# Kernel tuning notes

Hardware: AMD Instinct MI355X
Metric: run time of the kernel (lower is better)

The kernel has to match this reference:

```python
import jax, jax.numpy as jnp
import numpy as np

N, E, B, H, L, T = 50000, 800000, 1000, 256, 5, 128
BN_EPS = 1e-5

def _bn(x, g, b):
    # training-mode batchnorm over node axis, biased variance (torch semantics)
    mu = jnp.mean(x, axis=0)
    var = jnp.mean(jnp.square(x - mu), axis=0)
    return (x - mu) * jax.lax.rsqrt(var + BN_EPS) * g + b

def setup_inputs() -> dict:
    key = jax.random.key(0)
    ks = jax.random.split(key, 12)
    s = lambda fan: 1.0 / np.sqrt(fan)
    inp = {}
    inp["x_atom"] = jax.random.normal(ks[0], (N, 9), jnp.float32)
    inp["x_pe"] = jax.random.normal(ks[1], (N, 8), jnp.float32)
    inp["edge_index"] = jax.random.randint(ks[2], (2, E), 0, N, dtype=jnp.int64)
    inp["batch"] = jnp.sort(jax.random.randint(ks[3], (N,), 0, B, dtype=jnp.int64))
    inp["ae_w"] = jax.random.normal(ks[4], (9, H), jnp.float32) * s(9)
    inp["ae_b"] = jnp.zeros((H,), jnp.float32)
    inp["pe_w"] = jax.random.normal(ks[5], (8, H), jnp.float32) * s(8)
    inp["pe_b"] = jnp.zeros((H,), jnp.float32)
    inp["w1"] = jax.random.normal(ks[6], (L, H, H), jnp.float32) * s(H)
    inp["b1"] = jnp.zeros((L, H), jnp.float32)
    inp["g1"] = jnp.ones((L, H), jnp.float32)
    inp["be1"] = jnp.zeros((L, H), jnp.float32)
    inp["w2"] = jax.random.normal(ks[7], (L, H, H), jnp.float32) * s(H)
    inp["b2"] = jnp.zeros((L, H), jnp.float32)
    inp["bng"] = jnp.ones((L, H), jnp.float32)
    inp["bnb"] = jnp.zeros((L, H), jnp.float32)
    inp["cl1_w"] = jax.random.normal(ks[8], (H, H), jnp.float32) * s(H)
    inp["cl1_b"] = jnp.zeros((H,), jnp.float32)
    inp["clg"] = jnp.ones((H,), jnp.float32)
    inp["clb"] = jnp.zeros((H,), jnp.float32)
    inp["cl2_w"] = jax.random.normal(ks[9], (H, T), jnp.float32) * s(H)
    inp["cl2_b"] = jnp.zeros((T,), jnp.float32)
    return inp

def reference(x_atom, x_pe, edge_index, batch, ae_w, ae_b, pe_w, pe_b,
              w1, b1, g1, be1, w2, b2, bng, bnb,
              cl1_w, cl1_b, clg, clb, cl2_w, cl2_b):
    src, dst = edge_index[0], edge_index[1]
    h = x_atom @ ae_w + ae_b + x_pe @ pe_w + pe_b  # (N, H)
    for i in range(L):
        # GINConv (eps=0): (1+eps)*x + sum_{j in N(i)} x_j, then MLP
        agg = jax.ops.segment_sum(h[src], dst, num_segments=N)
        z = h + agg
        z = z @ w1[i] + b1[i]
        z = jax.nn.relu(_bn(z, g1[i], be1[i]))
        z = z @ w2[i] + b2[i]
        # outer BN + ReLU (dropout is identity in eval)
        h = jax.nn.relu(_bn(z, bng[i], bnb[i]))
    # global mean pool per graph
    sums = jax.ops.segment_sum(h, batch, num_segments=B)
    counts = jax.ops.segment_sum(jnp.ones((N,), h.dtype), batch, num_segments=B)
    pooled = sums / jnp.maximum(counts, 1.0)[:, None]  # (B, H)
    z = pooled @ cl1_w + cl1_b
    z = jax.nn.relu(_bn(z, clg, clb))
    logits = z @ cl2_w + cl2_b  # (B, T)
    return logits
```

## Files before the change

kernel.cpp:

```cpp
#include <hip/hip_runtime.h>
#include <hip/hip_bf16.h>
#include <stdint.h>

#define HH 256
#define BN_EPS 1e-5f
#define CHUNK 256
#define NSLOT 12

static inline int cdiv(int a, int b) { return (a + b - 1) / b; }

typedef _Float16 f16x8 __attribute__((ext_vector_type(8)));
typedef __attribute__((ext_vector_type(4))) float f32x4;

__device__ __forceinline__ unsigned short f2h(float f) {
    _Float16 h = (_Float16)f;
    unsigned short u;
    __builtin_memcpy(&u, &h, 2);
    return u;
}
__device__ __forceinline__ float h2f(unsigned short u) {
    _Float16 h;
    __builtin_memcpy(&h, &u, 2);
    return (float)h;
}

__device__ __forceinline__ void gload16(const void* g, void* lds) {
    __builtin_amdgcn_global_load_lds((const __attribute__((address_space(1))) unsigned int*)g,
                                     (__attribute__((address_space(3))) unsigned int*)lds, 16, 0, 0);
}

__device__ __forceinline__ void bn_derive(const float* __restrict__ stats, const float* __restrict__ g,
                                          const float* __restrict__ b, float invM, int c,
                                          float& sc, float& sh) {
    float mu = stats[c] * invM;
    float var = stats[HH + c] * invM - mu * mu;
    float rstd = rsqrtf(var + BN_EPS);
    sc = rstd * g[c];
    sh = b[c] - mu * sc;
}

__global__ void embed_kernel(const float* __restrict__ xa, const float* __restrict__ xp,
                             const float* __restrict__ aw, const float* __restrict__ ab,
                             const float* __restrict__ pw, const float* __restrict__ pb,
                             unsigned short* __restrict__ h, int N) {
    int n = blockIdx.x;
    int c = threadIdx.x;
    if (n >= N) return;
    float acc = ab[c] + pb[c];
#pragma unroll
    for (int k = 0; k < 9; ++k) acc += xa[n * 9 + k] * aw[k * HH + c];
#pragma unroll
    for (int k = 0; k < 8; ++k) acc += xp[n * 8 + k] * pw[k * HH + c];
    h[(size_t)n * HH + c] = f2h(acc);
}

__global__ void setup_kernel(int* __restrict__ deg, int N, float* __restrict__ stats) {
    int i = blockIdx.x * blockDim.x + threadIdx.x;
    if (i < N) deg[i] = 0;
    if (i < NSLOT * 512) {
        int slot = i >> 9;
        stats[(size_t)slot * 4 * HH + (i & 511)] = 0.f;
    }
}

__global__ void hist_kernel(const int* __restrict__ ei, int* __restrict__ deg, int E) {
    int e = blockIdx.x * blockDim.x + threadIdx.x;
    if (e < E) atomicAdd(&deg[ei[(size_t)E + e]], 1);
}

__global__ void ps1_kernel(const int* __restrict__ deg, int* __restrict__ chunkSum, int N) {
    __shared__ int sm[CHUNK];
    int i = blockIdx.x * CHUNK + threadIdx.x;
    sm[threadIdx.x] = (i < N) ? deg[i] : 0;
    __syncthreads();
    for (int off = CHUNK / 2; off > 0; off >>= 1) {
        if (threadIdx.x < off) sm[threadIdx.x] += sm[threadIdx.x + off];
        __syncthreads();
    }
    if (threadIdx.x == 0) chunkSum[blockIdx.x] = sm[0];
}

__global__ void ps2_kernel(const int* __restrict__ chunkSum, int* __restrict__ chunkOff,
                           int nc, int* __restrict__ offs, int N, int E) {
    __shared__ int sm[CHUNK];
    int t = threadIdx.x;
    int own = (t < nc) ? chunkSum[t] : 0;
    sm[t] = own;
    for (int off = 1; off < CHUNK; off <<= 1) {
        __syncthreads();
        int v = (t >= off) ? sm[t - off] : 0;
        __syncthreads();
        sm[t] += v;
    }
    if (t < nc) chunkOff[t] = sm[t] - own;
    if (t == 0) offs[N] = E;
}

__global__ void ps3_kernel(const int* __restrict__ deg, const int* __restrict__ chunkOff,
                           int* __restrict__ offs, int* __restrict__ cursor, int N) {
    __shared__ int sm[CHUNK];
    int t = threadIdx.x;
    int i = blockIdx.x * CHUNK + t;
    int own = (i < N) ? deg[i] : 0;
    sm[t] = own;
    for (int off = 1; off < CHUNK; off <<= 1) {
        __syncthreads();
        int v = (t >= off) ? sm[t - off] : 0;
        __syncthreads();
        sm[t] += v;
    }
    if (i < N) {
        int o = chunkOff[blockIdx.x] + sm[t] - own;
        offs[i] = o;
        cursor[i] = o;
    }
}

__global__ void fill_kernel(const int* __restrict__ ei, int* __restrict__ cursor,
                            int* __restrict__ srcl, int E) {
    int e = blockIdx.x * blockDim.x + threadIdx.x;
    if (e >= E) return;
    int s = ei[e];
    int d = ei[(size_t)E + e];
    int pos = atomicAdd(&cursor[d], 1);
    srcl[pos] = s;
}

__global__ void transpose_w_kernel(const float* __restrict__ W1, const float* __restrict__ W2,
                                   unsigned short* __restrict__ Wt1, unsigned short* __restrict__ Wt2,
                                   int perSet) {
    __shared__ float tile[32][33];
    int id = blockIdx.x;
    const float* W = W1;
    unsigned short* Wt = Wt1;
    if (id >= perSet) { W = W2; Wt = Wt2; id -= perSet; }
    int mat = id >> 6, t = id & 63;
    int kt = (t >> 3) * 32, nt = (t & 7) * 32;
    const float* Wm = W + (size_t)mat * HH * HH;
    unsigned short* Wtm = Wt + (size_t)mat * HH * HH;
    int lx = threadIdx.x & 31, ly = threadIdx.x >> 5;
#pragma unroll
    for (int yy = 0; yy < 32; yy += 8)
        tile[ly + yy][lx] = Wm[(size_t)(kt + ly + yy) * HH + nt + lx];
    __syncthreads();
#pragma unroll
    for (int yy = 0; yy < 32; yy += 8)
        Wtm[(size_t)(nt + ly + yy) * HH + kt + lx] = f2h(tile[lx][ly + yy]);
}

__global__ __launch_bounds__(256) void aggregate_fused_kernel(
        const unsigned short* __restrict__ h,
        const int* __restrict__ offs, const int* __restrict__ srcl,
        const float* __restrict__ stats, const float* __restrict__ gv,
        const float* __restrict__ bv, float invM,
        unsigned short* __restrict__ z, int N) {
    int n = blockIdx.x * 4 + (threadIdx.x >> 6);
    int l = threadIdx.x & 63;
    if (n >= N) return;
    int c = l * 4;
    const bool apply = (stats != nullptr);
    float sc0 = 1.f, sc1 = 1.f, sc2 = 1.f, sc3 = 1.f;
    float sh0 = 0.f, sh1 = 0.f, sh2 = 0.f, sh3 = 0.f;
    if (apply) {
        bn_derive(stats, gv, bv, invM, c + 0, sc0, sh0);
        bn_derive(stats, gv, bv, invM, c + 1, sc1, sh1);
        bn_derive(stats, gv, bv, invM, c + 2, sc2, sh2);
        bn_derive(stats, gv, bv, invM, c + 3, sc3, sh3);
    }

#define LOADT(row, r0, r1, r2, r3)                                      \
    {                                                                   \
        ushort4 v_ = *(const ushort4*)&h[(size_t)(row) * HH + c];       \
        r0 = h2f(v_.x); r1 = h2f(v_.y); r2 = h2f(v_.z); r3 = h2f(v_.w); \
        if (apply) {                                                    \
            r0 = fmaxf(r0 * sc0 + sh0, 0.f);                            \
            r1 = fmaxf(r1 * sc1 + sh1, 0.f);                            \
            r2 = fmaxf(r2 * sc2 + sh2, 0.f);                            \
            r3 = fmaxf(r3 * sc3 + sh3, 0.f);                            \
        }                                                               \
    }

    float a0, a1, a2, a3;
    LOADT(n, a0, a1, a2, a3);
    int s0 = offs[n], s1 = offs[n + 1];
    int j = s0;
    for (; j + 4 <= s1; j += 4) {
        int r0 = srcl[j], r1 = srcl[j + 1], r2 = srcl[j + 2], r3 = srcl[j + 3];
        float t0, t1, t2, t3, u0, u1, u2, u3;
        float p0, p1, p2, p3, q0, q1, q2, q3;
        LOADT(r0, t0, t1, t2, t3);
        LOADT(r1, u0, u1, u2, u3);
        LOADT(r2, p0, p1, p2, p3);
        LOADT(r3, q0, q1, q2, q3);
        a0 += (t0 + u0) + (p0 + q0);
        a1 += (t1 + u1) + (p1 + q1);
        a2 += (t2 + u2) + (p2 + q2);
        a3 += (t3 + u3) + (p3 + q3);
    }
    for (; j < s1; ++j) {
        float t0, t1, t2, t3;
        LOADT(srcl[j], t0, t1, t2, t3);
        a0 += t0; a1 += t1; a2 += t2; a3 += t3;
    }
#undef LOADT
    ushort4 o;
    o.x = f2h(a0); o.y = f2h(a1); o.z = f2h(a2); o.w = f2h(a3);
    *(ushort4*)&z[(size_t)n * HH + c] = o;
}

template <bool BN>
__global__ __launch_bounds__(256) void mfma_gemm_t(const unsigned short* __restrict__ A,
                                                   const unsigned short* __restrict__ Wt,
                                                   const float* __restrict__ bias,
                                                   unsigned short* __restrict__ C,
                                                   float* __restrict__ stats,
                                                   const float* __restrict__ bnstats,
                                                   const float* __restrict__ gv,
                                                   const float* __restrict__ bv,
                                                   float invM, int M) {
    __shared__ unsigned short sm[128 * 136];
    __shared__ __align__(16) _Float16 lsc[256];
    __shared__ __align__(16) _Float16 lsh[256];
    __shared__ float sred[256];
    unsigned short* As = sm;
    unsigned short* Bs = sm + 128 * 64;
    int tid = threadIdx.x;
    int w = tid >> 6, l = tid & 63;
    int wr = w >> 1, wc = w & 1;

    int nRow = (M + 127) >> 7;
    int fullIds = (nRow & ~7) * 2;
    int id = blockIdx.x;
    int p, cc;
    if (id < fullIds) {
        int gq = id >> 4, r = id & 15;
        cc = r >> 3;
        p = gq * 8 + (r & 7);
    } else {
        int t = id - fullIds;
        p = (nRow & ~7) + (t >> 1);
        cc = t & 1;
    }
    int row0 = p * 128;
    int col0 = cc * 128;

    int g = (l & 7) ^ (l >> 3);
    int srow = w * 8 + (l >> 3);

    if (BN) {
        float sc, sh;
        bn_derive(bnstats, gv, bv, invM, tid, sc, sh);
        lsc[tid] = (_Float16)sc;
        lsh[tid] = (_Float16)sh;
        __syncthreads();
    }

    f32x4 acc[4][4] = {};

    const unsigned short* AB = A + (size_t)row0 * HH;
    const unsigned short* WB = Wt + (size_t)col0 * HH;

    for (int k0 = 0; k0 < 256; k0 += 64) {
#pragma unroll
        for (int r = 0; r < 4; ++r) {
            int row = r * 32 + srow;
            size_t go = (size_t)row * HH + k0 + g * 8;
            int lo = (r * 32 + w * 8) * 64;
            gload16(AB + go, &As[lo]);
            gload16(WB + go, &Bs[lo]);
        }
        __syncthreads();
#pragma unroll
        for (int kh = 0; kh < 2; ++kh) {
            f16x8 af[4], bf[4];
            f16x8 scv, shv;
            if (BN) {
                int kb = k0 + (kh * 4 + (l >> 4)) * 8;
                scv = *(const f16x8*)&lsc[kb];
                shv = *(const f16x8*)&lsh[kb];
            }
#pragma unroll
            for (int m = 0; m < 4; ++m) {
                int rr = wr * 64 + m * 16 + (l & 15);
                int gs = (kh * 4 + (l >> 4)) ^ (rr & 7);
                af[m] = *(const f16x8*)&As[rr * 64 + gs * 8];
                if (BN) {
                    af[m] = af[m] * scv + shv;
                    af[m] = __builtin_elementwise_max(af[m], (f16x8)(_Float16)0);
                }
            }
#pragma unroll
            for (int n = 0; n < 4; ++n) {
                int rr = wc * 64 + n * 16 + (l & 15);
                int gs = (kh * 4 + (l >> 4)) ^ (rr & 7);
                bf[n] = *(const f16x8*)&Bs[rr * 64 + gs * 8];
            }
#pragma unroll
            for (int m = 0; m < 4; ++m)
#pragma unroll
                for (int n = 0; n < 4; ++n)
                    acc[m][n] = __builtin_amdgcn_mfma_f32_16x16x32_f16(af[m], bf[n], acc[m][n], 0, 0, 0);
        }
        __syncthreads();
    }

    int mvalid = M - row0;
    float sv[4], s2v[4];
#pragma unroll
    for (int n = 0; n < 4; ++n) {
        int colr = wc * 64 + n * 16 + (l & 15);
        float bvv = bias[col0 + colr];
        float s = 0.f, s2 = 0.f;
#pragma unroll
        for (int m = 0; m < 4; ++m) {
            int rb = wr * 64 + m * 16 + (l >> 4) * 4;
#pragma unroll
            for (int r = 0; r < 4; ++r) {
                float v = acc[m][n][r] + bvv;
                sm[(rb + r) * 136 + colr] = f2h(v);
                if (rb + r < mvalid) { s += v; s2 += v * v; }
            }
        }
        s += __shfl_xor(s, 16);   s += __shfl_xor(s, 32);
        s2 += __shfl_xor(s2, 16); s2 += __shfl_xor(s2, 32);
        sv[n] = s;
        s2v[n] = s2;
    }
    if (wr == 1 && (l >> 4) == 0) {
#pragma unroll
        for (int n = 0; n < 4; ++n) {
            int colr = wc * 64 + n * 16 + (l & 15);
            sred[colr] = sv[n];
            sred[128 + colr] = s2v[n];
        }
    }
    __syncthreads();
    if (wr == 0 && (l >> 4) == 0) {
#pragma unroll
        for (int n = 0; n < 4; ++n) {
            int colr = wc * 64 + n * 16 + (l & 15);
            atomicAdd(&stats[col0 + colr], sv[n] + sred[colr]);
            atomicAdd(&stats[HH + col0 + colr], s2v[n] + sred[128 + colr]);
        }
    }
#pragma unroll
    for (int i = 0; i < 8; ++i) {
        int ci = i * 256 + tid;
        int row = ci >> 4;
        int cq = (ci & 15) * 8;
        if (row0 + row < M) {
            uint4 v = *(const uint4*)&sm[row * 136 + cq];
            *(uint4*)&C[(size_t)(row0 + row) * HH + col0 + cq] = v;
        }
    }
}

__global__ void bn_stats_kernel(const float* __restrict__ X, int M, float* __restrict__ stats) {
    int c = threadIdx.x;
    int r0 = blockIdx.x * 128;
    int r1 = min(r0 + 128, M);
    float s = 0.f, s2 = 0.f;
    for (int r = r0; r < r1; ++r) {
        float v = X[(size_t)r * HH + c];
        s += v;
        s2 += v * v;
    }
    atomicAdd(&stats[c], s);
    atomicAdd(&stats[HH + c], s2);
}

__global__ void bn_finalize_kernel(float* __restrict__ stats, const float* __restrict__ g,
                                   const float* __restrict__ b, float invM) {
    int c = threadIdx.x;
    float sc, sh;
    bn_derive(stats, g, b, invM, c, sc, sh);
    stats[2 * HH + c] = sc;
    stats[3 * HH + c] = sh;
}

__global__ void bn_apply_relu_kernel(float* __restrict__ X, int n4, const float* __restrict__ stats) {
    int i = blockIdx.x * blockDim.x + threadIdx.x;
    int stride = gridDim.x * blockDim.x;
    for (; i < n4; i += stride) {
        int c4 = (i & 63) * 4;
        float4 v = ((float4*)X)[i];
        float4 sc = *(const float4*)&stats[2 * HH + c4];
        float4 sh = *(const float4*)&stats[3 * HH + c4];
        v.x = fmaxf(v.x * sc.x + sh.x, 0.f);
        v.y = fmaxf(v.y * sc.y + sh.y, 0.f);
        v.z = fmaxf(v.z * sc.z + sh.z, 0.f);
        v.w = fmaxf(v.w * sc.w + sh.w, 0.f);
        ((float4*)X)[i] = v;
    }
}

__global__ __launch_bounds__(256) void gemm_kernel(const float* __restrict__ A,
                                                   const float* __restrict__ W,
                                                   const float* __restrict__ bias,
                                                   float* __restrict__ C,
                                                   int M, int ldw) {
    __shared__ float Asm[64][33];
    __shared__ float Wsm[32][64];
    int tid = threadIdx.x;
    int tx = tid & 15, ty = tid >> 4;
    int row0 = blockIdx.x * 64;
    int col0 = blockIdx.y * 64;
    float acc[4][4] = {};

    for (int k0 = 0; k0 < 256; k0 += 32) {
#pragma unroll
        for (int t = 0; t < 2; ++t) {
            int s = tid + t * 256;
            int m = s >> 3;
            int kq = (s & 7) * 4;
            float4 v = make_float4(0.f, 0.f, 0.f, 0.f);
            if (row0 + m < M) v = *(const float4*)&A[(size_t)(row0 + m) * 256 + k0 + kq];
            Asm[m][kq + 0] = v.x; Asm[m][kq + 1] = v.y; Asm[m][kq + 2] = v.z; Asm[m][kq + 3] = v.w;
        }
#pragma unroll
        for (int t = 0; t < 2; ++t) {
            int s = tid + t * 256;
            int kk = s >> 4;
            int cq = (s & 15) * 4;
            *(float4*)&Wsm[kk][cq] = *(const float4*)&W[(size_t)(k0 + kk) * ldw + col0 + cq];
        }
        __syncthreads();
#pragma unroll
        for (int kk = 0; kk < 32; ++kk) {
            float a0 = Asm[ty * 4 + 0][kk];
            float a1 = Asm[ty * 4 + 1][kk];
            float a2 = Asm[ty * 4 + 2][kk];
            float a3 = Asm[ty * 4 + 3][kk];
            float4 wv = *(const float4*)&Wsm[kk][tx * 4];
            acc[0][0] += a0 * wv.x; acc[0][1] += a0 * wv.y; acc[0][2] += a0 * wv.z; acc[0][3] += a0 * wv.w;
            acc[1][0] += a1 * wv.x; acc[1][1] += a1 * wv.y; acc[1][2] += a1 * wv.z; acc[1][3] += a1 * wv.w;
            acc[2][0] += a2 * wv.x; acc[2][1] += a2 * wv.y; acc[2][2] += a2 * wv.z; acc[2][3] += a2 * wv.w;
            acc[3][0] += a3 * wv.x; acc[3][1] += a3 * wv.y; acc[3][2] += a3 * wv.z; acc[3][3] += a3 * wv.w;
        }
        __syncthreads();
    }

    float4 bvv = *(const float4*)&bias[col0 + tx * 4];
#pragma unroll
    for (int j = 0; j < 4; ++j) {
        int row = row0 + ty * 4 + j;
        if (row < M) {
            float4 o = make_float4(acc[j][0] + bvv.x, acc[j][1] + bvv.y,
                                   acc[j][2] + bvv.z, acc[j][3] + bvv.w);
            *(float4*)&C[(size_t)row * ldw + col0 + tx * 4] = o;
        }
    }
}

__device__ __forceinline__ int lbound(const int* a, int n, int v) {
    int lo = 0, hi = n;
    while (lo < hi) {
        int mid = (lo + hi) >> 1;
        if (a[mid] < v) lo = mid + 1; else hi = mid;
    }
    return lo;
}

__global__ void pool_fused_kernel(const unsigned short* __restrict__ Hm,
                                  const int* __restrict__ batch,
                                  const float* __restrict__ stats,
                                  const float* __restrict__ gv,
                                  const float* __restrict__ bv, float invM,
                                  int N, float* __restrict__ pooled) {
    int g = blockIdx.x;
    int c = threadIdx.x;
    int s = lbound(batch, N, g);
    int e = lbound(batch, N, g + 1);
    float sc, sh;
    bn_derive(stats, gv, bv, invM, c, sc, sh);
    float acc = 0.f;
    for (int r = s; r < e; ++r)
        acc += fmaxf(h2f(Hm[(size_t)r * HH + c]) * sc + sh, 0.f);
    pooled[(size_t)g * HH + c] = acc / (float)max(e - s, 1);
}

extern "C" void kernel_launch(void* const* d_in, const int* in_sizes, int n_in,
                              void* d_out, int out_size, void* d_ws, size_t ws_size,
                              hipStream_t stream) {
    const float* x_atom = (const float*)d_in[0];
    const float* x_pe   = (const float*)d_in[1];
    const int* ei       = (const int*)d_in[2];
    const int* batch    = (const int*)d_in[3];
    const float* ae_w = (const float*)d_in[4];
    const float* ae_b = (const float*)d_in[5];
    const float* pe_w = (const float*)d_in[6];
    const float* pe_b = (const float*)d_in[7];
    const float* w1  = (const float*)d_in[8];
    const float* b1  = (const float*)d_in[9];
    const float* g1  = (const float*)d_in[10];
    const float* be1 = (const float*)d_in[11];
    const float* w2  = (const float*)d_in[12];
    const float* b2  = (const float*)d_in[13];
    const float* bng = (const float*)d_in[14];
    const float* bnb = (const float*)d_in[15];
    const float* cl1_w = (const float*)d_in[16];
    const float* cl1_b = (const float*)d_in[17];
    const float* clg = (const float*)d_in[18];
    const float* clb = (const float*)d_in[19];
    const float* cl2_w = (const float*)d_in[20];
    const float* cl2_b = (const float*)d_in[21];

    const int N = in_sizes[3];
    const int E = in_sizes[2] / 2;
    const int T = in_sizes[21];
    const int B = out_size / T;
    const int Lnum = in_sizes[9] / HH;
    const int nc = cdiv(N, CHUNK);
    const int Npad = cdiv(N, 128) * 128;
    const size_t P = (size_t)Npad * HH;

    unsigned short* X = (unsigned short*)d_ws;
    unsigned short* Y = X + P;
    unsigned short* wt1 = Y + P;
    unsigned short* wt2 = wt1 + (size_t)Lnum * HH * HH;
    float* stats = (float*)(wt2 + (size_t)Lnum * HH * HH);
    float* pooled = stats + (size_t)NSLOT * 4 * HH;
    float* zc = pooled + (size_t)B * HH;
    int* deg = (int*)(zc + (size_t)B * HH);
    int* offs = deg + N;
    int* cursor = offs + N + 1;
    int* chunkSum = cursor + N;
    int* chunkOff = chunkSum + 256;
    int* srcl = chunkOff + 256;

    const int BH4 = B * (HH / 4);
    const float invN = 1.f / (float)N;

    setup_kernel<<<cdiv(max(N, NSLOT * 512), 256), 256, 0, stream>>>(deg, N, stats);

    hist_kernel<<<cdiv(E, 256), 256, 0, stream>>>(ei, deg, E);
    ps1_kernel<<<nc, CHUNK, 0, stream>>>(deg, chunkSum, N);
    ps2_kernel<<<1, CHUNK, 0, stream>>>(chunkSum, chunkOff, nc, offs, N, E);
    ps3_kernel<<<nc, CHUNK, 0, stream>>>(deg, chunkOff, offs, cursor, N);
    fill_kernel<<<cdiv(E, 256), 256, 0, stream>>>(ei, cursor, srcl, E);

    transpose_w_kernel<<<2 * Lnum * 64, 256, 0, stream>>>(w1, w2, wt1, wt2, Lnum * 64);

    embed_kernel<<<N, HH, 0, stream>>>(x_atom, x_pe, ae_w, ae_b, pe_w, pe_b, X, N);

    const int nRow = cdiv(N, 128);
    const int mf_blocks = 2 * nRow;

    unsigned short *in = X, *ot = Y;

    for (int i = 0; i < Lnum; ++i) {
        float* slot1 = stats + (size_t)(2 * i) * 4 * HH;
        float* slot2 = stats + (size_t)(2 * i + 1) * 4 * HH;
        const float* aggStats = (i == 0) ? nullptr : stats + (size_t)(2 * i - 1) * 4 * HH;
        const float* aggG = (i == 0) ? nullptr : bng + (size_t)(i - 1) * HH;
        const float* aggB = (i == 0) ? nullptr : bnb + (size_t)(i - 1) * HH;

        aggregate_fused_kernel<<<cdiv(N, 4), 256, 0, stream>>>(in, offs, srcl,
                                                               aggStats, aggG, aggB, invN, ot, N);

        mfma_gemm_t<false><<<mf_blocks, 256, 0, stream>>>(ot, wt1 + (size_t)i * HH * HH,
                                                          b1 + (size_t)i * HH, in, slot1,
                                                          nullptr, nullptr, nullptr, 0.f, N);

        mfma_gemm_t<true><<<mf_blocks, 256, 0, stream>>>(in, wt2 + (size_t)i * HH * HH,
                                                         b2 + (size_t)i * HH, ot, slot2,
                                                         slot1, g1 + (size_t)i * HH,
                                                         be1 + (size_t)i * HH, invN, N);

        unsigned short* t = in; in = ot; ot = t;
    }

    pool_fused_kernel<<<B, HH, 0, stream>>>(in, batch,
                                            stats + (size_t)(2 * Lnum - 1) * 4 * HH,
                                            bng + (size_t)(Lnum - 1) * HH,
                                            bnb + (size_t)(Lnum - 1) * HH, invN, N, pooled);

    float* slotC = stats + (size_t)10 * 4 * HH;
    dim3 cls_grid1(cdiv(B, 64), HH / 64);
    gemm_kernel<<<cls_grid1, 256, 0, stream>>>(pooled, cl1_w, cl1_b, zc, B, HH);
    bn_stats_kernel<<<cdiv(B, 128), HH, 0, stream>>>(zc, B, slotC);
    bn_finalize_kernel<<<1, HH, 0, stream>>>(slotC, clg, clb, 1.f / B);
    bn_apply_relu_kernel<<<min(2048, cdiv(BH4, 256)), 256, 0, stream>>>(zc, BH4, slotC);

    dim3 cls_grid2(cdiv(B, 64), T / 64);
    gemm_kernel<<<cls_grid2, 256, 0, stream>>>(zc, cl2_w, cl2_b, (float*)d_out, B, T);
}
```

Measured before the change: 888.6 us.

## Vectorize embedding, unroll aggregation by eight, fuse classifier BN stats into GEMM

Three separate changes. The embedding kernel now handles four nodes per 256-thread block, with each lane computing four channels using float4 weight loads and a ushort4 store. The neighbour aggregation loop gains an 8-way unrolled path so more gather loads are in flight at once. The classifier BN statistics are accumulated in the first GEMM epilogue with shuffles and atomics, and scale/shift are derived inline in the apply kernel, which removes two kernel launches. The cost is more register pressure in the aggregation kernel and repeated per-element BN derivation.

```diff
diff --git a/kernel.cpp b/kernel.cpp
--- a/kernel.cpp
+++ b/kernel.cpp
@@ -39,19 +39,35 @@
     sh = b[c] - mu * sc;
 }
 
-__global__ void embed_kernel(const float* __restrict__ xa, const float* __restrict__ xp,
-                             const float* __restrict__ aw, const float* __restrict__ ab,
-                             const float* __restrict__ pw, const float* __restrict__ pb,
-                             unsigned short* __restrict__ h, int N) {
-    int n = blockIdx.x;
-    int c = threadIdx.x;
+__global__ __launch_bounds__(256) void embed_kernel(const float* __restrict__ xa,
+                                                    const float* __restrict__ xp,
+                                                    const float* __restrict__ aw,
+                                                    const float* __restrict__ ab,
+                                                    const float* __restrict__ pw,
+                                                    const float* __restrict__ pb,
+                                                    unsigned short* __restrict__ h, int N) {
+    int n = blockIdx.x * 4 + (threadIdx.x >> 6);
+    int l = threadIdx.x & 63;
     if (n >= N) return;
-    float acc = ab[c] + pb[c];
-#pragma unroll
-    for (int k = 0; k < 9; ++k) acc += xa[n * 9 + k] * aw[k * HH + c];
-#pragma unroll
-    for (int k = 0; k < 8; ++k) acc += xp[n * 8 + k] * pw[k * HH + c];
-    h[(size_t)n * HH + c] = f2h(acc);
+    int c = l * 4;
+    float4 abv = *(const float4*)&ab[c];
+    float4 pbv = *(const float4*)&pb[c];
+    float a0 = abv.x + pbv.x, a1 = abv.y + pbv.y, a2 = abv.z + pbv.z, a3 = abv.w + pbv.w;
+#pragma unroll
+    for (int k = 0; k < 9; ++k) {
+        float xv = xa[n * 9 + k];
+        float4 w = *(const float4*)&aw[k * HH + c];
+        a0 += xv * w.x; a1 += xv * w.y; a2 += xv * w.z; a3 += xv * w.w;
+    }
+#pragma unroll
+    for (int k = 0; k < 8; ++k) {
+        float xv = xp[n * 8 + k];
+        float4 w = *(const float4*)&pw[k * HH + c];
+        a0 += xv * w.x; a1 += xv * w.y; a2 += xv * w.z; a3 += xv * w.w;
+    }
+    ushort4 o;
+    o.x = f2h(a0); o.y = f2h(a1); o.z = f2h(a2); o.w = f2h(a3);
+    *(ushort4*)&h[(size_t)n * HH + c] = o;
 }
 
 __global__ void setup_kernel(int* __restrict__ deg, int N, float* __restrict__ stats) {
@@ -184,18 +200,34 @@
     LOADT(n, a0, a1, a2, a3);
     int s0 = offs[n], s1 = offs[n + 1];
     int j = s0;
+    for (; j + 8 <= s1; j += 8) {
+        int r0 = srcl[j], r1 = srcl[j + 1], r2 = srcl[j + 2], r3 = srcl[j + 3];
+        int r4 = srcl[j + 4], r5 = srcl[j + 5], r6 = srcl[j + 6], r7 = srcl[j + 7];
+        float t0[4], t1[4], t2[4], t3[4], t4[4], t5[4], t6[4], t7[4];
+        LOADT(r0, t0[0], t0[1], t0[2], t0[3]);
+        LOADT(r1, t1[0], t1[1], t1[2], t1[3]);
+        LOADT(r2, t2[0], t2[1], t2[2], t2[3]);
+        LOADT(r3, t3[0], t3[1], t3[2], t3[3]);
+        LOADT(r4, t4[0], t4[1], t4[2], t4[3]);
+        LOADT(r5, t5[0], t5[1], t5[2], t5[3]);
+        LOADT(r6, t6[0], t6[1], t6[2], t6[3]);
+        LOADT(r7, t7[0], t7[1], t7[2], t7[3]);
+        a0 += ((t0[0] + t1[0]) + (t2[0] + t3[0])) + ((t4[0] + t5[0]) + (t6[0] + t7[0]));
+        a1 += ((t0[1] + t1[1]) + (t2[1] + t3[1])) + ((t4[1] + t5[1]) + (t6[1] + t7[1]));
+        a2 += ((t0[2] + t1[2]) + (t2[2] + t3[2])) + ((t4[2] + t5[2]) + (t6[2] + t7[2]));
+        a3 += ((t0[3] + t1[3]) + (t2[3] + t3[3])) + ((t4[3] + t5[3]) + (t6[3] + t7[3]));
+    }
     for (; j + 4 <= s1; j += 4) {
         int r0 = srcl[j], r1 = srcl[j + 1], r2 = srcl[j + 2], r3 = srcl[j + 3];
-        float t0, t1, t2, t3, u0, u1, u2, u3;
-        float p0, p1, p2, p3, q0, q1, q2, q3;
-        LOADT(r0, t0, t1, t2, t3);
-        LOADT(r1, u0, u1, u2, u3);
-        LOADT(r2, p0, p1, p2, p3);
-        LOADT(r3, q0, q1, q2, q3);
-        a0 += (t0 + u0) + (p0 + q0);
-        a1 += (t1 + u1) + (p1 + q1);
-        a2 += (t2 + u2) + (p2 + q2);
-        a3 += (t3 + u3) + (p3 + q3);
+        float t0[4], t1[4], t2[4], t3[4];
+        LOADT(r0, t0[0], t0[1], t0[2], t0[3]);
+        LOADT(r1, t1[0], t1[1], t1[2], t1[3]);
+        LOADT(r2, t2[0], t2[1], t2[2], t2[3]);
+        LOADT(r3, t3[0], t3[1], t3[2], t3[3]);
+        a0 += (t0[0] + t1[0]) + (t2[0] + t3[0]);
+        a1 += (t0[1] + t1[1]) + (t2[1] + t3[1]);
+        a2 += (t0[2] + t1[2]) + (t2[2] + t3[2]);
+        a3 += (t0[3] + t1[3]) + (t2[3] + t3[3]);
     }
     for (; j < s1; ++j) {
         float t0, t1, t2, t3;
@@ -355,50 +387,13 @@
     }
 }
 
-__global__ void bn_stats_kernel(const float* __restrict__ X, int M, float* __restrict__ stats) {
-    int c = threadIdx.x;
-    int r0 = blockIdx.x * 128;
-    int r1 = min(r0 + 128, M);
-    float s = 0.f, s2 = 0.f;
-    for (int r = r0; r < r1; ++r) {
-        float v = X[(size_t)r * HH + c];
-        s += v;
-        s2 += v * v;
-    }
-    atomicAdd(&stats[c], s);
-    atomicAdd(&stats[HH + c], s2);
-}
-
-__global__ void bn_finalize_kernel(float* __restrict__ stats, const float* __restrict__ g,
-                                   const float* __restrict__ b, float invM) {
-    int c = threadIdx.x;
-    float sc, sh;
-    bn_derive(stats, g, b, invM, c, sc, sh);
-    stats[2 * HH + c] = sc;
-    stats[3 * HH + c] = sh;
-}
-
-__global__ void bn_apply_relu_kernel(float* __restrict__ X, int n4, const float* __restrict__ stats) {
-    int i = blockIdx.x * blockDim.x + threadIdx.x;
-    int stride = gridDim.x * blockDim.x;
-    for (; i < n4; i += stride) {
-        int c4 = (i & 63) * 4;
-        float4 v = ((float4*)X)[i];
-        float4 sc = *(const float4*)&stats[2 * HH + c4];
-        float4 sh = *(const float4*)&stats[3 * HH + c4];
-        v.x = fmaxf(v.x * sc.x + sh.x, 0.f);
-        v.y = fmaxf(v.y * sc.y + sh.y, 0.f);
-        v.z = fmaxf(v.z * sc.z + sh.z, 0.f);
-        v.w = fmaxf(v.w * sc.w + sh.w, 0.f);
-        ((float4*)X)[i] = v;
-    }
-}
-
-__global__ __launch_bounds__(256) void gemm_kernel(const float* __restrict__ A,
-                                                   const float* __restrict__ W,
-                                                   const float* __restrict__ bias,
-                                                   float* __restrict__ C,
-                                                   int M, int ldw) {
+template <bool ST>
+__global__ __launch_bounds__(256) void gemm_t(const float* __restrict__ A,
+                                              const float* __restrict__ W,
+                                              const float* __restrict__ bias,
+                                              float* __restrict__ C,
+                                              float* __restrict__ stats,
+                                              int M, int ldw) {
     __shared__ float Asm[64][33];
     __shared__ float Wsm[32][64];
     int tid = threadIdx.x;
@@ -441,6 +436,7 @@
     }
 
     float4 bvv = *(const float4*)&bias[col0 + tx * 4];
+    float s[4] = {}, s2[4] = {};
 #pragma unroll
     for (int j = 0; j < 4; ++j) {
         int row = row0 + ty * 4 + j;
@@ -448,7 +444,45 @@
             float4 o = make_float4(acc[j][0] + bvv.x, acc[j][1] + bvv.y,
                                    acc[j][2] + bvv.z, acc[j][3] + bvv.w);
             *(float4*)&C[(size_t)row * ldw + col0 + tx * 4] = o;
-        }
+            if (ST) {
+                s[0] += o.x; s2[0] += o.x * o.x;
+                s[1] += o.y; s2[1] += o.y * o.y;
+                s[2] += o.z; s2[2] += o.z * o.z;
+                s[3] += o.w; s2[3] += o.w * o.w;
+            }
+        }
+    }
+    if (ST) {
+#pragma unroll
+        for (int q = 0; q < 4; ++q) {
+            s[q] += __shfl_xor(s[q], 16);  s[q] += __shfl_xor(s[q], 32);
+            s2[q] += __shfl_xor(s2[q], 16); s2[q] += __shfl_xor(s2[q], 32);
+        }
+        if (((tid & 63) >> 4) == 0) {
+#pragma unroll
+            for (int q = 0; q < 4; ++q) {
+                atomicAdd(&stats[col0 + tx * 4 + q], s[q]);
+                atomicAdd(&stats[HH + col0 + tx * 4 + q], s2[q]);
+            }
+        }
+    }
+}
+
+__global__ void bn_apply_relu_kernel(float* __restrict__ X, int n4,
+                                     const float* __restrict__ stats,
+                                     const float* __restrict__ gv,
+                                     const float* __restrict__ bv, float invM) {
+    int i = blockIdx.x * blockDim.x + threadIdx.x;
+    int stride = gridDim.x * blockDim.x;
+    for (; i < n4; i += stride) {
+        int c4 = (i & 63) * 4;
+        float4 v = ((float4*)X)[i];
+        float sc, sh;
+        bn_derive(stats, gv, bv, invM, c4 + 0, sc, sh); v.x = fmaxf(v.x * sc + sh, 0.f);
+        bn_derive(stats, gv, bv, invM, c4 + 1, sc, sh); v.y = fmaxf(v.y * sc + sh, 0.f);
+        bn_derive(stats, gv, bv, invM, c4 + 2, sc, sh); v.z = fmaxf(v.z * sc + sh, 0.f);
+        bn_derive(stats, gv, bv, invM, c4 + 3, sc, sh); v.w = fmaxf(v.w * sc + sh, 0.f);
+        ((float4*)X)[i] = v;
     }
 }
 
@@ -541,7 +575,7 @@
 
     transpose_w_kernel<<<2 * Lnum * 64, 256, 0, stream>>>(w1, w2, wt1, wt2, Lnum * 64);
 
-    embed_kernel<<<N, HH, 0, stream>>>(x_atom, x_pe, ae_w, ae_b, pe_w, pe_b, X, N);
+    embed_kernel<<<cdiv(N, 4), 256, 0, stream>>>(x_atom, x_pe, ae_w, ae_b, pe_w, pe_b, X, N);
 
     const int nRow = cdiv(N, 128);
     const int mf_blocks = 2 * nRow;
@@ -577,11 +611,10 @@
 
     float* slotC = stats + (size_t)10 * 4 * HH;
     dim3 cls_grid1(cdiv(B, 64), HH / 64);
-    gemm_kernel<<<cls_grid1, 256, 0, stream>>>(pooled, cl1_w, cl1_b, zc, B, HH);
-    bn_stats_kernel<<<cdiv(B, 128), HH, 0, stream>>>(zc, B, slotC);
-    bn_finalize_kernel<<<1, HH, 0, stream>>>(slotC, clg, clb, 1.f / B);
-    bn_apply_relu_kernel<<<min(2048, cdiv(BH4, 256)), 256, 0, stream>>>(zc, BH4, slotC);
+    gemm_t<true><<<cls_grid1, 256, 0, stream>>>(pooled, cl1_w, cl1_b, zc, slotC, B, HH);
+    bn_apply_relu_kernel<<<min(2048, cdiv(BH4, 256)), 256, 0, stream>>>(zc, BH4, slotC,
+                                                                        clg, clb, 1.f / B);
 
     dim3 cls_grid2(cdiv(B, 64), T / 64);
-    gemm_kernel<<<cls_grid2, 256, 0, stream>>>(zc, cl2_w, cl2_b, (float*)d_out, B, T);
-}
+    gemm_t<false><<<cls_grid2, 256, 0, stream>>>(zc, cl2_w, cl2_b, (float*)d_out, nullptr, B, T);
+}
```

New measurement: 843.8 us. -5.0%, faster.
